# Optimization experiments

Measured on AMD Instinct MI355X. Metric: run time of the kernel, lower is better.

Reference implementation:

```python
import jax, jax.numpy as jnp
import numpy as np


def _chamfer_single_directional(x, y):
    """Mean over batch of mean over points of min_j ||x_i - y_j||^2.

    x: [B, N, 3] (predicted), y: [B, M, 3] (target).
    Matches pytorch3d chamfer_distance(x, y, single_directional=True)
    with norm=2, point_reduction='mean', batch_reduction='mean'.
    """
    x2 = jnp.sum(x * x, axis=-1)                      # [B, N]
    y2 = jnp.sum(y * y, axis=-1)                      # [B, M]
    cross = jnp.einsum('bnd,bmd->bnm', x, y)          # [B, N, M]
    d2 = x2[:, :, None] + y2[:, None, :] - 2.0 * cross  # squared L2
    min_d2 = jnp.min(d2, axis=2)                      # [B, N] nearest in y
    return jnp.mean(jnp.mean(min_d2, axis=1))         # scalar


def setup_inputs() -> dict:
    key = jax.random.key(0)
    k1, k2 = jax.random.split(key)
    v = jax.random.normal(k1, (4, 8192, 3), dtype=jnp.float32)
    v_pred = jax.random.normal(k2, (4, 8192, 3), dtype=jnp.float32)
    return {"v": v, "v_pred": v_pred}


def reference(v, v_pred):
    # forward: chamfer_distance(v_pred, v, single_directional=True)
    return _chamfer_single_directional(v_pred, v)
```

## Files before the change

### kernel.cpp

```cpp
#include <hip/hip_runtime.h>

#define BB 4
#define NN 8192
#define MM 8192
#define BN (BB * NN)

#define BLK 256
#define QB  256
#define TC  1024
#define SCH (MM / TC)
#define NJT (TC / 32)

#define KEY_C 128.0f

typedef __bf16 bf16x8 __attribute__((ext_vector_type(8)));
typedef float  f32x16 __attribute__((ext_vector_type(16)));


static __device__ inline void split_bf(float v, __bf16& h, __bf16& l) {
    h = (__bf16)v;
    l = (__bf16)(v - (float)h);
}

__global__ __launch_bounds__(BLK) void chamfer_mfma(
    const float* __restrict__ y,
    const float* __restrict__ x,
    int* __restrict__ gkey)
{
    __shared__ uint4 FR[NJT * 64];

    const int t  = threadIdx.x;
    const int l  = t & 63;
    const int w  = t >> 6;
    const int ib = blockIdx.x;
    const int s  = blockIdx.y;
    const int b  = blockIdx.z;

    {
        const float* xb = x + ((size_t)b * NN + (size_t)ib * QB) * 3;
        float x0 = xb[3*t+0], x1 = xb[3*t+1], x2 = xb[3*t+2];
        __bf16 h0,l0,h1,l1,h2,l2;
        split_bf(2.0f*x0, h0, l0);
        split_bf(2.0f*x1, h1, l1);
        split_bf(2.0f*x2, h2, l2);
        float nxx = -__builtin_fmaf(x2, x2, __builtin_fmaf(x1, x1, x0*x0));
        __bf16 hx, lx; split_bf(nxx, hx, lx);
        const __bf16 one = (__bf16)1.0f;
        bf16x8 g0 = {h0,h0,l0,l0,h1,h1,l1,l1};
        bf16x8 g1 = {h2,h2,l2,l2,hx,lx,one,one};
        const int at = t >> 5, col = t & 31;
        FR[at*64 +      col] = __builtin_bit_cast(uint4, g0);
        FR[at*64 + 32 + col] = __builtin_bit_cast(uint4, g1);
    }
    __syncthreads();
    const bf16x8 a0 = __builtin_bit_cast(bf16x8, FR[(w*2 + 0)*64 + l]);
    const bf16x8 a1 = __builtin_bit_cast(bf16x8, FR[(w*2 + 1)*64 + l]);
    __syncthreads();

    {
        const float* yb = y + ((size_t)b * MM + (size_t)s * TC) * 3;
        const __bf16 one = (__bf16)1.0f;
#pragma unroll
        for (int k2 = 0; k2 < 4; ++k2) {
            const int j = t + k2 * BLK;
            float y0 = yb[3*j+0], y1 = yb[3*j+1], y2 = yb[3*j+2];
            __bf16 h0,l0,h1,l1,h2,l2;
            split_bf(y0, h0, l0);
            split_bf(y1, h1, l1);
            split_bf(y2, h2, l2);
            float nyy = -__builtin_fmaf(y2, y2, __builtin_fmaf(y1, y1, y0*y0));
            __bf16 hy, ly; split_bf(nyy, hy, ly);
            bf16x8 g0 = {h0,l0,h0,l0,h1,l1,h1,l1};
            bf16x8 g1 = {h2,l2,h2,l2,one,one,hy,ly};
            const int jt = j >> 5, col = j & 31;
            FR[jt*64 +      col] = __builtin_bit_cast(uint4, g0);
            FR[jt*64 + 32 + col] = __builtin_bit_cast(uint4, g1);
        }
    }
    __syncthreads();

    f32x16 ck;
#pragma unroll
    for (int r = 0; r < 16; ++r) ck[r] = KEY_C;
    f32x16 best0, best1;
#pragma unroll
    for (int r = 0; r < 16; ++r) { best0[r] = -3.4e38f; best1[r] = -3.4e38f; }

#pragma unroll 1
    for (int jt = 0; jt < NJT; jt += 2) {
        const bf16x8 bf0 = __builtin_bit_cast(bf16x8, FR[jt*64 + l]);
        const bf16x8 bf1 = __builtin_bit_cast(bf16x8, FR[jt*64 + 64 + l]);
        f32x16 p = __builtin_amdgcn_mfma_f32_32x32x16_bf16(a0, bf0, ck, 0, 0, 0);
        f32x16 q = __builtin_amdgcn_mfma_f32_32x32x16_bf16(a0, bf1, ck, 0, 0, 0);
#pragma unroll
        for (int r = 0; r < 16; ++r)
            best0[r] = fmaxf(fmaxf(best0[r], p[r]), q[r]);
        f32x16 u = __builtin_amdgcn_mfma_f32_32x32x16_bf16(a1, bf0, ck, 0, 0, 0);
        f32x16 v2 = __builtin_amdgcn_mfma_f32_32x32x16_bf16(a1, bf1, ck, 0, 0, 0);
#pragma unroll
        for (int r = 0; r < 16; ++r)
            best1[r] = fmaxf(fmaxf(best1[r], u[r]), v2[r]);
    }

    int* gk = gkey + (size_t)b * NN + (size_t)ib * QB;
    const int g = l >> 5;
#pragma unroll
    for (int ii = 0; ii < 2; ++ii) {
        const f32x16 bb = ii ? best1 : best0;
#pragma unroll
        for (int r = 0; r < 16; ++r) {
            float v = bb[r];
            v = fmaxf(v, __shfl_xor(v, 1, 64));
            v = fmaxf(v, __shfl_xor(v, 2, 64));
            v = fmaxf(v, __shfl_xor(v, 4, 64));
            v = fmaxf(v, __shfl_xor(v, 8, 64));
            v = fmaxf(v, __shfl_xor(v, 16, 64));
            if ((l & 31) == 0) {
                const int row = (r & 3) + 8 * (r >> 2) + 4 * g;
                atomicMax(&gk[(w*2 + ii)*32 + row], __float_as_int(v));
            }
        }
    }
}

__global__ __launch_bounds__(1024) void final_sum(
    const int* __restrict__ gkey,
    float* __restrict__ out)
{
    const int t = threadIdx.x;
    const int4* g4 = (const int4*)gkey;
    float acc = 0.0f;
#pragma unroll
    for (int i = t; i < BN / 4; i += 1024) {
        int4 k = g4[i];
        acc += (KEY_C - __int_as_float(k.x)) + (KEY_C - __int_as_float(k.y))
             + (KEY_C - __int_as_float(k.z)) + (KEY_C - __int_as_float(k.w));
    }
    for (int off = 32; off > 0; off >>= 1) {
        acc += __shfl_down(acc, off, 64);
    }
    __shared__ float wsum[16];
    const int lane = t & 63;
    const int w    = t >> 6;
    if (lane == 0) wsum[w] = acc;
    __syncthreads();
    if (t == 0) {
        float tot = 0.0f;
#pragma unroll
        for (int i = 0; i < 16; ++i) tot += wsum[i];
        out[0] = tot * (1.0f / (float)BN);
    }
}

extern "C" void kernel_launch(void* const* d_in, const int* in_sizes, int n_in,
                              void* d_out, int out_size, void* d_ws, size_t ws_size,
                              hipStream_t stream) {
    const float* v      = (const float*)d_in[0];
    const float* v_pred = (const float*)d_in[1];
    float* out = (float*)d_out;

    int* gkey = (int*)d_ws;

    dim3 grid1(NN / QB, SCH, BB);
    chamfer_mfma<<<grid1, BLK, 0, stream>>>(v, v_pred, gkey);

    final_sum<<<1, 1024, 0, stream>>>(gkey, out);
}
```

Before: 76.10 us.

## Prepack bf16 split fragments globally and fuse final reduction via last-block atomics

Adds a prepack kernel that converts x and y once into MFMA-ready hi/lo bf16 fragments in the workspace. The main kernel then streams y fragments straight from global/L2 instead of rebuilding them per block in shared memory. Each 512-thread block now covers 64 queries against all of M, with 8 waves splitting the y range and reducing through shared memory rather than global atomicMax. The separate final_sum launch is replaced by per-block atomicAdd partials and a last-block-done counter. This removes redundant conversion work and a kernel launch, but the inner loop now depends on global-load latency and the float atomic sum order is nondeterministic.

```diff
diff --git a/kernel.cpp b/kernel.cpp
--- a/kernel.cpp
+++ b/kernel.cpp
@@ -5,13 +5,10 @@
 #define MM 8192
 #define BN (BB * NN)
 
-#define BLK 256
-#define QB  256
-#define TC  1024
-#define SCH (MM / TC)
-#define NJT (TC / 32)
-
-#define KEY_C 128.0f
+#define QB   64
+#define CBLK 512
+#define NBLK ((NN / QB) * BB)
+#define JTW  (MM / 32 / 8)
 
 typedef __bf16 bf16x8 __attribute__((ext_vector_type(8)));
 typedef float  f32x16 __attribute__((ext_vector_type(16)));
@@ -22,91 +19,98 @@
     l = (__bf16)(v - (float)h);
 }
 
-__global__ __launch_bounds__(BLK) void chamfer_mfma(
+__global__ __launch_bounds__(256) void prepack(
+    const float* __restrict__ x,
     const float* __restrict__ y,
-    const float* __restrict__ x,
-    int* __restrict__ gkey)
+    uint4* __restrict__ ws4,
+    float* __restrict__ sums,
+    int* __restrict__ cnt)
 {
-    __shared__ uint4 FR[NJT * 64];
+    const int id  = blockIdx.x * 256 + threadIdx.x;
+    const int isB = blockIdx.y;
 
-    const int t  = threadIdx.x;
-    const int l  = t & 63;
-    const int w  = t >> 6;
-    const int ib = blockIdx.x;
-    const int s  = blockIdx.y;
-    const int b  = blockIdx.z;
+    if (blockIdx.x == 0 && isB == 0 && threadIdx.x < 17) {
+        if (threadIdx.x < 16) sums[threadIdx.x] = 0.0f;
+        else *cnt = 0;
+    }
 
-    {
-        const float* xb = x + ((size_t)b * NN + (size_t)ib * QB) * 3;
-        float x0 = xb[3*t+0], x1 = xb[3*t+1], x2 = xb[3*t+2];
+    const float* s = isB ? y : x;
+    float c0 = s[3*id+0], c1 = s[3*id+1], c2 = s[3*id+2];
+    float nss = -__builtin_fmaf(c2, c2, __builtin_fmaf(c1, c1, c0*c0));
+    __bf16 sh, sl; split_bf(nss, sh, sl);
+    const __bf16 one = (__bf16)1.0f;
+    bf16x8 g0, g1;
+    if (!isB) {
         __bf16 h0,l0,h1,l1,h2,l2;
-        split_bf(2.0f*x0, h0, l0);
-        split_bf(2.0f*x1, h1, l1);
-        split_bf(2.0f*x2, h2, l2);
-        float nxx = -__builtin_fmaf(x2, x2, __builtin_fmaf(x1, x1, x0*x0));
-        __bf16 hx, lx; split_bf(nxx, hx, lx);
-        const __bf16 one = (__bf16)1.0f;
-        bf16x8 g0 = {h0,h0,l0,l0,h1,h1,l1,l1};
-        bf16x8 g1 = {h2,h2,l2,l2,hx,lx,one,one};
-        const int at = t >> 5, col = t & 31;
-        FR[at*64 +      col] = __builtin_bit_cast(uint4, g0);
-        FR[at*64 + 32 + col] = __builtin_bit_cast(uint4, g1);
+        split_bf(2.0f*c0, h0, l0);
+        split_bf(2.0f*c1, h1, l1);
+        split_bf(2.0f*c2, h2, l2);
+        g0 = bf16x8{h0,h0,l0,l0,h1,h1,l1,l1};
+        g1 = bf16x8{h2,h2,l2,l2,sh,sl,one,one};
+    } else {
+        __bf16 h0,l0,h1,l1,h2,l2;
+        split_bf(c0, h0, l0);
+        split_bf(c1, h1, l1);
+        split_bf(c2, h2, l2);
+        g0 = bf16x8{h0,l0,h0,l0,h1,l1,h1,l1};
+        g1 = bf16x8{h2,l2,h2,l2,one,one,sh,sl};
     }
-    __syncthreads();
-    const bf16x8 a0 = __builtin_bit_cast(bf16x8, FR[(w*2 + 0)*64 + l]);
-    const bf16x8 a1 = __builtin_bit_cast(bf16x8, FR[(w*2 + 1)*64 + l]);
-    __syncthreads();
+    uint4* dst = ws4 + (size_t)(isB ? BN*2 : 0);
+    const int base = (id >> 5) * 64 + (id & 31);
+    dst[base]      = __builtin_bit_cast(uint4, g0);
+    dst[base + 32] = __builtin_bit_cast(uint4, g1);
+}
 
-    {
-        const float* yb = y + ((size_t)b * MM + (size_t)s * TC) * 3;
-        const __bf16 one = (__bf16)1.0f;
+__global__ __launch_bounds__(CBLK, 4) void chamfer(
+    const uint4* __restrict__ ws4,
+    float* __restrict__ out,
+    float* __restrict__ sums,
+    int* __restrict__ cnt)
+{
+    const int t   = threadIdx.x;
+    const int l   = t & 63;
+    const int w   = t >> 6;
+    const int hi  = l >> 5;
+    const int c32 = l & 31;
+    const int ib  = blockIdx.x;
+    const int b   = blockIdx.y;
+
+    const uint4* xf = ws4;
+    const uint4* yf = ws4 + (size_t)BN * 2;
+
+    const int xtile = b * (NN/32) + ib * 2;
+    const bf16x8 a0 = __builtin_bit_cast(bf16x8, xf[(size_t)xtile*64 + hi*32 + c32]);
+    const bf16x8 a1 = __builtin_bit_cast(bf16x8, xf[(size_t)(xtile+1)*64 + hi*32 + c32]);
+
+    const uint4* yb = yf + ((size_t)b * (MM/32) + w * JTW) * 64 + hi*32 + c32;
+
+    f32x16 z;
 #pragma unroll
-        for (int k2 = 0; k2 < 4; ++k2) {
-            const int j = t + k2 * BLK;
-            float y0 = yb[3*j+0], y1 = yb[3*j+1], y2 = yb[3*j+2];
-            __bf16 h0,l0,h1,l1,h2,l2;
-            split_bf(y0, h0, l0);
-            split_bf(y1, h1, l1);
-            split_bf(y2, h2, l2);
-            float nyy = -__builtin_fmaf(y2, y2, __builtin_fmaf(y1, y1, y0*y0));
-            __bf16 hy, ly; split_bf(nyy, hy, ly);
-            bf16x8 g0 = {h0,l0,h0,l0,h1,l1,h1,l1};
-            bf16x8 g1 = {h2,l2,h2,l2,one,one,hy,ly};
-            const int jt = j >> 5, col = j & 31;
-            FR[jt*64 +      col] = __builtin_bit_cast(uint4, g0);
-            FR[jt*64 + 32 + col] = __builtin_bit_cast(uint4, g1);
-        }
-    }
-    __syncthreads();
-
-    f32x16 ck;
-#pragma unroll
-    for (int r = 0; r < 16; ++r) ck[r] = KEY_C;
+    for (int r = 0; r < 16; ++r) z[r] = 0.0f;
     f32x16 best0, best1;
 #pragma unroll
     for (int r = 0; r < 16; ++r) { best0[r] = -3.4e38f; best1[r] = -3.4e38f; }
 
 #pragma unroll 1
-    for (int jt = 0; jt < NJT; jt += 2) {
-        const bf16x8 bf0 = __builtin_bit_cast(bf16x8, FR[jt*64 + l]);
-        const bf16x8 bf1 = __builtin_bit_cast(bf16x8, FR[jt*64 + 64 + l]);
-        f32x16 p = __builtin_amdgcn_mfma_f32_32x32x16_bf16(a0, bf0, ck, 0, 0, 0);
-        f32x16 q = __builtin_amdgcn_mfma_f32_32x32x16_bf16(a0, bf1, ck, 0, 0, 0);
+    for (int jt = 0; jt < JTW; jt += 2) {
+        const bf16x8 bf0 = __builtin_bit_cast(bf16x8, yb[(size_t)jt * 64]);
+        const bf16x8 bf1 = __builtin_bit_cast(bf16x8, yb[(size_t)jt * 64 + 64]);
+        f32x16 p = __builtin_amdgcn_mfma_f32_32x32x16_bf16(a0, bf0, z, 0, 0, 0);
+        f32x16 q = __builtin_amdgcn_mfma_f32_32x32x16_bf16(a0, bf1, z, 0, 0, 0);
 #pragma unroll
         for (int r = 0; r < 16; ++r)
             best0[r] = fmaxf(fmaxf(best0[r], p[r]), q[r]);
-        f32x16 u = __builtin_amdgcn_mfma_f32_32x32x16_bf16(a1, bf0, ck, 0, 0, 0);
-        f32x16 v2 = __builtin_amdgcn_mfma_f32_32x32x16_bf16(a1, bf1, ck, 0, 0, 0);
+        p = __builtin_amdgcn_mfma_f32_32x32x16_bf16(a1, bf0, z, 0, 0, 0);
+        q = __builtin_amdgcn_mfma_f32_32x32x16_bf16(a1, bf1, z, 0, 0, 0);
 #pragma unroll
         for (int r = 0; r < 16; ++r)
-            best1[r] = fmaxf(fmaxf(best1[r], u[r]), v2[r]);
+            best1[r] = fmaxf(fmaxf(best1[r], p[r]), q[r]);
     }
 
-    int* gk = gkey + (size_t)b * NN + (size_t)ib * QB;
-    const int g = l >> 5;
+    __shared__ float red[8][QB];
 #pragma unroll
-    for (int ii = 0; ii < 2; ++ii) {
-        const f32x16 bb = ii ? best1 : best0;
+    for (int at = 0; at < 2; ++at) {
+        const f32x16 bb = at ? best1 : best0;
 #pragma unroll
         for (int r = 0; r < 16; ++r) {
             float v = bb[r];
@@ -115,40 +119,38 @@
             v = fmaxf(v, __shfl_xor(v, 4, 64));
             v = fmaxf(v, __shfl_xor(v, 8, 64));
             v = fmaxf(v, __shfl_xor(v, 16, 64));
-            if ((l & 31) == 0) {
-                const int row = (r & 3) + 8 * (r >> 2) + 4 * g;
-                atomicMax(&gk[(w*2 + ii)*32 + row], __float_as_int(v));
+            if (c32 == 0) {
+                const int R = (r & 3) + 8 * (r >> 2) + 4 * hi;
+                red[w][at * 32 + R] = v;
             }
         }
     }
-}
+    __syncthreads();
 
-__global__ __launch_bounds__(1024) void final_sum(
-    const int* __restrict__ gkey,
-    float* __restrict__ out)
-{
-    const int t = threadIdx.x;
-    const int4* g4 = (const int4*)gkey;
-    float acc = 0.0f;
+    if (w == 0) {
+        float m = red[0][l];
 #pragma unroll
-    for (int i = t; i < BN / 4; i += 1024) {
-        int4 k = g4[i];
-        acc += (KEY_C - __int_as_float(k.x)) + (KEY_C - __int_as_float(k.y))
-             + (KEY_C - __int_as_float(k.z)) + (KEY_C - __int_as_float(k.w));
-    }
-    for (int off = 32; off > 0; off >>= 1) {
-        acc += __shfl_down(acc, off, 64);
-    }
-    __shared__ float wsum[16];
-    const int lane = t & 63;
-    const int w    = t >> 6;
-    if (lane == 0) wsum[w] = acc;
-    __syncthreads();
-    if (t == 0) {
-        float tot = 0.0f;
-#pragma unroll
-        for (int i = 0; i < 16; ++i) tot += wsum[i];
-        out[0] = tot * (1.0f / (float)BN);
+        for (int k = 1; k < 8; ++k) m = fmaxf(m, red[k][l]);
+        float part = -m;
+        for (int off = 32; off > 0; off >>= 1)
+            part += __shfl_down(part, off, 64);
+
+        int old = 0;
+        if (l == 0) {
+            atomicAdd(&sums[(ib * BB + b) & 15], part);
+            __threadfence();
+            old = atomicAdd(cnt, 1);
+        }
+        old = __shfl(old, 0, 64);
+        if (old == NBLK - 1) {
+            float tot = 0.0f;
+            if (l < 16) tot = atomicAdd(&sums[l], 0.0f);
+            tot += __shfl_down(tot, 8, 64);
+            tot += __shfl_down(tot, 4, 64);
+            tot += __shfl_down(tot, 2, 64);
+            tot += __shfl_down(tot, 1, 64);
+            if (l == 0) out[0] = tot * (1.0f / (float)BN);
+        }
     }
 }
 
@@ -159,10 +161,10 @@
     const float* v_pred = (const float*)d_in[1];
     float* out = (float*)d_out;
 
-    int* gkey = (int*)d_ws;
+    uint4* ws4   = (uint4*)d_ws;
+    float* sums  = (float*)((char*)d_ws + ((size_t)BN * 4) * 16);
+    int*   cnt   = (int*)(sums + 16);
 
-    dim3 grid1(NN / QB, SCH, BB);
-    chamfer_mfma<<<grid1, BLK, 0, stream>>>(v, v_pred, gkey);
-
-    final_sum<<<1, 1024, 0, stream>>>(gkey, out);
+    prepack<<<dim3(BN / 256, 2), 256, 0, stream>>>(v_pred, v, ws4, sums, cnt);
+    chamfer<<<dim3(NN / QB, BB), CBLK, 0, stream>>>(ws4, out, sums, cnt);
 }
```

Result: slower. 82.49 us (+8.4%).

## Fuse final reduction into chamfer kernel via last-block-done counters

Applied to the files above, without the earlier changes.

Removes the separate final_sum launch. Each block now writes its per-query partial maxima into a per-split slot with plain stores, replacing the atomicMax on integer keys. A per-group counter picks the last-arriving block, which takes the min across splits, reduces its group, and adds the result to a global total. A second counter then lets the last group write the output. This saves a kernel launch and the atomic contention, at the cost of extra fences and counters whose correctness depends on the workspace being zeroed before each call (the probe offset P is read from it but never written).

```diff
diff --git a/kernel.cpp b/kernel.cpp
--- a/kernel.cpp
+++ b/kernel.cpp
@@ -8,13 +8,13 @@
 #define BLK 256
 #define QB  256
 #define TC  1024
-#define SCH (MM / TC)
+#define S   (MM / TC)
 #define NJT (TC / 32)
-
-#define KEY_C 128.0f
+#define NGRP ((NN / QB) * BB)
 
 typedef __bf16 bf16x8 __attribute__((ext_vector_type(8)));
 typedef float  f32x16 __attribute__((ext_vector_type(16)));
+
 
 
 static __device__ inline void split_bf(float v, __bf16& h, __bf16& l) {
@@ -22,19 +22,31 @@
     l = (__bf16)(v - (float)h);
 }
 
-__global__ __launch_bounds__(BLK) void chamfer_mfma(
+__global__ __launch_bounds__(BLK, 4) void chamfer_one(
     const float* __restrict__ y,
     const float* __restrict__ x,
-    int* __restrict__ gkey)
+    float* __restrict__ part,
+    int*   __restrict__ group_cnt,
+    float* __restrict__ total,
+    int*   __restrict__ gcnt,
+    const int* __restrict__ probe,
+    float* __restrict__ out)
 {
     __shared__ uint4 FR[NJT * 64];
+    __shared__ int   lastFlag;
+    __shared__ float wsum[4];
 
-    const int t  = threadIdx.x;
-    const int l  = t & 63;
-    const int w  = t >> 6;
-    const int ib = blockIdx.x;
-    const int s  = blockIdx.y;
-    const int b  = blockIdx.z;
+    const int t   = threadIdx.x;
+    const int l   = t & 63;
+    const int w   = t >> 6;
+    const int hi  = l >> 5;
+    const int c32 = l & 31;
+    const int ib  = blockIdx.x;
+    const int s   = blockIdx.y;
+    const int b   = blockIdx.z;
+    const int g   = b * (NN / QB) + ib;
+
+    const int P = *probe;
 
     {
         const float* xb = x + ((size_t)b * NN + (size_t)ib * QB) * 3;
@@ -79,9 +91,9 @@
     }
     __syncthreads();
 
-    f32x16 ck;
+    f32x16 z;
 #pragma unroll
-    for (int r = 0; r < 16; ++r) ck[r] = KEY_C;
+    for (int r = 0; r < 16; ++r) z[r] = 0.0f;
     f32x16 best0, best1;
 #pragma unroll
     for (int r = 0; r < 16; ++r) { best0[r] = -3.4e38f; best1[r] = -3.4e38f; }
@@ -90,20 +102,19 @@
     for (int jt = 0; jt < NJT; jt += 2) {
         const bf16x8 bf0 = __builtin_bit_cast(bf16x8, FR[jt*64 + l]);
         const bf16x8 bf1 = __builtin_bit_cast(bf16x8, FR[jt*64 + 64 + l]);
-        f32x16 p = __builtin_amdgcn_mfma_f32_32x32x16_bf16(a0, bf0, ck, 0, 0, 0);
-        f32x16 q = __builtin_amdgcn_mfma_f32_32x32x16_bf16(a0, bf1, ck, 0, 0, 0);
+        f32x16 p = __builtin_amdgcn_mfma_f32_32x32x16_bf16(a0, bf0, z, 0, 0, 0);
+        f32x16 q = __builtin_amdgcn_mfma_f32_32x32x16_bf16(a0, bf1, z, 0, 0, 0);
 #pragma unroll
         for (int r = 0; r < 16; ++r)
             best0[r] = fmaxf(fmaxf(best0[r], p[r]), q[r]);
-        f32x16 u = __builtin_amdgcn_mfma_f32_32x32x16_bf16(a1, bf0, ck, 0, 0, 0);
-        f32x16 v2 = __builtin_amdgcn_mfma_f32_32x32x16_bf16(a1, bf1, ck, 0, 0, 0);
+        p = __builtin_amdgcn_mfma_f32_32x32x16_bf16(a1, bf0, z, 0, 0, 0);
+        q = __builtin_amdgcn_mfma_f32_32x32x16_bf16(a1, bf1, z, 0, 0, 0);
 #pragma unroll
         for (int r = 0; r < 16; ++r)
-            best1[r] = fmaxf(fmaxf(best1[r], u[r]), v2[r]);
+            best1[r] = fmaxf(fmaxf(best1[r], p[r]), q[r]);
     }
 
-    int* gk = gkey + (size_t)b * NN + (size_t)ib * QB;
-    const int g = l >> 5;
+    float* pslot = part + ((size_t)g * S + s) * QB;
 #pragma unroll
     for (int ii = 0; ii < 2; ++ii) {
         const f32x16 bb = ii ? best1 : best0;
@@ -115,40 +126,48 @@
             v = fmaxf(v, __shfl_xor(v, 4, 64));
             v = fmaxf(v, __shfl_xor(v, 8, 64));
             v = fmaxf(v, __shfl_xor(v, 16, 64));
-            if ((l & 31) == 0) {
-                const int row = (r & 3) + 8 * (r >> 2) + 4 * g;
-                atomicMax(&gk[(w*2 + ii)*32 + row], __float_as_int(v));
+            if (c32 == 0) {
+                const int qrow = (w*2 + ii)*32 + (r & 3) + 8*(r >> 2) + 4*hi;
+                __hip_atomic_store(&pslot[qrow], -v, __ATOMIC_RELAXED,
+                                   __HIP_MEMORY_SCOPE_AGENT);
             }
         }
     }
-}
 
-__global__ __launch_bounds__(1024) void final_sum(
-    const int* __restrict__ gkey,
-    float* __restrict__ out)
-{
-    const int t = threadIdx.x;
-    const int4* g4 = (const int4*)gkey;
-    float acc = 0.0f;
+    __threadfence();
+    if (t == 0) {
+        int old = atomicAdd(&group_cnt[g], 1);
+        lastFlag = (old == P + S - 1);
+    }
+    __syncthreads();
+    if (!lastFlag) return;
+
+    __threadfence();
+    const float* pg = part + (size_t)g * S * QB;
+    float dq = 3.4e38f;
 #pragma unroll
-    for (int i = t; i < BN / 4; i += 1024) {
-        int4 k = g4[i];
-        acc += (KEY_C - __int_as_float(k.x)) + (KEY_C - __int_as_float(k.y))
-             + (KEY_C - __int_as_float(k.z)) + (KEY_C - __int_as_float(k.w));
+    for (int ss = 0; ss < S; ++ss) {
+        float vv = __hip_atomic_load(&pg[ss * QB + t], __ATOMIC_RELAXED,
+                                     __HIP_MEMORY_SCOPE_AGENT);
+        dq = fminf(dq, vv);
     }
-    for (int off = 32; off > 0; off >>= 1) {
+    float acc = dq;
+    for (int off = 32; off > 0; off >>= 1)
         acc += __shfl_down(acc, off, 64);
-    }
-    __shared__ float wsum[16];
-    const int lane = t & 63;
-    const int w    = t >> 6;
-    if (lane == 0) wsum[w] = acc;
+    if ((t & 63) == 0) wsum[t >> 6] = acc;
     __syncthreads();
     if (t == 0) {
-        float tot = 0.0f;
-#pragma unroll
-        for (int i = 0; i < 16; ++i) tot += wsum[i];
-        out[0] = tot * (1.0f / (float)BN);
+        float Sg = wsum[0] + wsum[1] + wsum[2] + wsum[3];
+        atomicAdd(total, Sg);
+        __threadfence();
+        int old2 = atomicAdd(gcnt, 1);
+        if (old2 == P + NGRP - 1) {
+            __threadfence();
+            float tot = __hip_atomic_load(total, __ATOMIC_RELAXED,
+                                          __HIP_MEMORY_SCOPE_AGENT);
+            tot -= __int_as_float(P);
+            out[0] = tot * (1.0f / (float)BN);
+        }
     }
 }
 
@@ -159,10 +178,13 @@
     const float* v_pred = (const float*)d_in[1];
     float* out = (float*)d_out;
 
-    int* gkey = (int*)d_ws;
+    char* wsb = (char*)d_ws;
+    float* part      = (float*)wsb;
+    int*   group_cnt = (int*)(wsb + (1u << 20));
+    float* total     = (float*)(wsb + (1u << 20) + 512);
+    int*   gcnt      = (int*)(wsb + (1u << 20) + 516);
+    int*   probe     = (int*)(wsb + (1u << 20) + 520);
 
-    dim3 grid1(NN / QB, SCH, BB);
-    chamfer_mfma<<<grid1, BLK, 0, stream>>>(v, v_pred, gkey);
-
-    final_sum<<<1, 1024, 0, stream>>>(gkey, out);
+    chamfer_one<<<dim3(NN / QB, S, BB), BLK, 0, stream>>>(
+        v, v_pred, part, group_cnt, total, gcnt, probe, out);
 }
```

New measurement: 134.7 us. +76.9%, slower.
